# Optimization experiments

Hardware: AMD Instinct MI355X
Metric: run time of the kernel (lower is better)

Reference implementation:

```python
import jax, jax.numpy as jnp
import numpy as np

B, L, DIM = 16, 131072, 9  # batch, audio samples, 1 fundamental + 8 harmonics
SR = 22050.0
SINE_AMP = 0.1
NOISE_STD = 0.003


def setup_inputs() -> dict:
    key = jax.random.key(0)
    k1, k2, k3, k4 = jax.random.split(key, 4)
    u = jax.random.uniform(k1, (B, L, 1), dtype=jnp.float32)
    voiced = jax.random.uniform(k2, (B, L, 1), dtype=jnp.float32) > 0.3
    f0 = jnp.where(voiced, 100.0 + 300.0 * u, 0.0)  # Hz, 0 where unvoiced
    rand_ini = jax.random.uniform(k3, (B, DIM), dtype=jnp.float32)
    rand_ini = rand_ini.at[:, 0].set(0.0)  # first harmonic gets no random phase
    noise_z = jax.random.normal(k4, (B, L, DIM), dtype=jnp.float32)
    return {"f0": f0, "rand_ini": rand_ini, "noise_z": noise_z}


def reference(f0, rand_ini, noise_z):
    dim = noise_z.shape[-1]
    two_pi = 2.0 * jnp.pi
    # harmonic multiples of f0: (B, L, dim)
    k = jnp.arange(1, dim + 1, dtype=f0.dtype)
    fn = f0 * k
    # normalized per-step phase increment in [0, 1)
    rad = jnp.mod(fn / SR, 1.0)
    rad = rad.at[:, 0, :].add(rand_ini)  # random initial phase per harmonic
    # wrap-around detection: cumulative phase mod 1 decreases at a wrap
    tmp_over_one = jnp.mod(jnp.cumsum(rad, axis=1), 1.0)
    wrap = (tmp_over_one[:, 1:, :] - tmp_over_one[:, :-1, :]) < 0.0
    cumsum_shift = jnp.concatenate(
        [jnp.zeros_like(rad[:, :1, :]), jnp.where(wrap, -1.0, 0.0).astype(rad.dtype)],
        axis=1,
    )
    sines = jnp.sin(jnp.cumsum(rad + cumsum_shift, axis=1) * two_pi)
    sine_waves = sines * SINE_AMP
    # voiced/unvoiced mask from fundamental f0
    uv = (f0 > 0.0).astype(f0.dtype)  # (B, L, 1)
    noise_amp = uv * NOISE_STD + (1.0 - uv) * (SINE_AMP / 3.0)
    noise = noise_amp * noise_z
    sine_waves = sine_waves * uv + noise
    return sine_waves, uv, noise
```

## Files before the change

### kernel.cpp

```cpp
#include <hip/hip_runtime.h>
#include <math.h>


#define Bq 16
#define Lq 131072
#define DIMq 9
#define CHUNK 2048
#define NCHUNK (Lq / CHUNK)
#define NTHREADS 256
#define PER_THREAD (CHUNK / NTHREADS)

static __device__ __forceinline__ int pad9(int p) { return p + (p >> 3); }

__global__ void __launch_bounds__(NTHREADS) k_partials(
    const float* __restrict__ f0, double* __restrict__ part) {
  int b = blockIdx.x / NCHUNK, c = blockIdx.x % NCHUNK;
  const float* p = f0 + (size_t)b * Lq + (size_t)c * CHUNK;
  double s = 0.0;
#pragma unroll
  for (int j = 0; j < PER_THREAD; ++j) s += (double)p[j * NTHREADS + threadIdx.x];
  __shared__ double sd[NTHREADS];
  sd[threadIdx.x] = s;
  __syncthreads();
  for (int off = NTHREADS / 2; off > 0; off >>= 1) {
    if (threadIdx.x < off) sd[threadIdx.x] += sd[threadIdx.x + off];
    __syncthreads();
  }
  if (threadIdx.x == 0) part[blockIdx.x] = sd[0];
}

__global__ void k_scan(double* __restrict__ part) {
  if (threadIdx.x == 0) {
    double run = 0.0;
    double* p = part + (size_t)blockIdx.x * NCHUNK;
    for (int c = 0; c < NCHUNK; ++c) { double v = p[c]; p[c] = run; run += v; }
  }
}

__global__ void __launch_bounds__(NTHREADS) k_main(
    const float* __restrict__ f0, const float* __restrict__ rini,
    const float* __restrict__ nz, const double* __restrict__ pref,
    float* __restrict__ out0, float* __restrict__ out1, float* __restrict__ out2) {
  int b = blockIdx.x / NCHUNK, c = blockIdx.x % NCHUNK;
  int tid = threadIdx.x;
  size_t rowbase = (size_t)b * Lq + (size_t)c * CHUNK;

  __shared__ float f0s[CHUNK + CHUNK / 8];
  __shared__ double Cl[CHUNK + CHUNK / 8];
  __shared__ double sd[NTHREADS];

#pragma unroll
  for (int j = 0; j < PER_THREAD; ++j) {
    int p = j * NTHREADS + tid;
    f0s[pad9(p)] = f0[rowbase + p];
  }
  __syncthreads();

  double run = 0.0;
  double inc[PER_THREAD];
#pragma unroll
  for (int j = 0; j < PER_THREAD; ++j) {
    run += (double)f0s[pad9(tid * PER_THREAD + j)];
    inc[j] = run;
  }
  sd[tid] = run;
  __syncthreads();
#pragma unroll
  for (int off = 1; off < NTHREADS; off <<= 1) {
    double v = (tid >= off) ? sd[tid - off] : 0.0;
    __syncthreads();
    sd[tid] += v;
    __syncthreads();
  }
  double base = pref[blockIdx.x] + (sd[tid] - run);
#pragma unroll
  for (int j = 0; j < PER_THREAD; ++j)
    Cl[pad9(tid * PER_THREAD + j)] = base + inc[j];
  __syncthreads();

  float ini[DIMq];
#pragma unroll
  for (int d = 0; d < DIMq; ++d) ini[d] = rini[b * DIMq + d];

  const double invsr = 1.0 / 22050.0;
  const float nampU = (float)(0.1 / 3.0);

  for (int j = 0; j < PER_THREAD; ++j) {
    int p = j * NTHREADS + tid;
    size_t t = rowbase + p;
    float f = f0s[pad9(p)];
    bool v = f > 0.0f;
    out1[t] = v ? 1.0f : 0.0f;
    double x = Cl[pad9(p)] * invsr;
    float namp = v ? 0.003f : nampU;
    const float* nzp = nz + t * DIMq;
    float* o0 = out0 + t * DIMq;
    float* o2 = out2 + t * DIMq;
#pragma unroll
    for (int d = 0; d < DIMq; ++d) {
      float nzv = nzp[d];
      float noise = namp * nzv;
      double ph = x * (double)(d + 1) + (double)ini[d];
      ph -= floor(ph);
      float s = __builtin_amdgcn_sinf((float)ph) * 0.1f;
      o2[d] = noise;
      o0[d] = v ? (s + noise) : noise;
    }
  }
}

extern "C" void kernel_launch(void* const* d_in, const int* in_sizes, int n_in,
                              void* d_out, int out_size, void* d_ws, size_t ws_size,
                              hipStream_t stream) {
  const float* f0 = (const float*)d_in[0];
  const float* rini = (const float*)d_in[1];
  const float* nz = (const float*)d_in[2];
  float* out = (float*)d_out;
  float* out0 = out;
  float* out1 = out + (size_t)Bq * Lq * DIMq;
  float* out2 = out1 + (size_t)Bq * Lq;
  double* part = (double*)d_ws;

  k_partials<<<Bq * NCHUNK, NTHREADS, 0, stream>>>(f0, part);
  k_scan<<<Bq, 64, 0, stream>>>(part);
  k_main<<<Bq * NCHUNK, NTHREADS, 0, stream>>>(f0, rini, nz, part,
                                               out0, out1, out2);
}
```

Measured before the change: 53.97 us.

## Vectorize noise I/O, drop scan kernel, use wave shuffles and float harmonic phases

Removes the serial k_scan launch by having each k_main block sum the preceding chunk partials with a wave reduction. Block-level shared-memory scans and reductions become wave shuffles. Each per-sample phase is reduced mod 1 in double once, and the nine harmonic phases are then computed in float. The 9-wide noise input and both 9-wide outputs are read and written as coalesced float4 over a flat index instead of strided scalar accesses. The float harmonic-phase step reduces precision slightly, since the value multiplied by up to 9 is already a float.

```diff
diff --git a/kernel.cpp b/kernel.cpp
--- a/kernel.cpp
+++ b/kernel.cpp
@@ -7,105 +7,109 @@
 #define DIMq 9
 #define CHUNK 2048
 #define NCHUNK (Lq / CHUNK)
-#define NTHREADS 256
-#define PER_THREAD (CHUNK / NTHREADS)
+#define NT 256
+#define PT 8
+#define Q4 (CHUNK * DIMq / 4 / NT)
 
-static __device__ __forceinline__ int pad9(int p) { return p + (p >> 3); }
-
-__global__ void __launch_bounds__(NTHREADS) k_partials(
-    const float* __restrict__ f0, double* __restrict__ part) {
-  int b = blockIdx.x / NCHUNK, c = blockIdx.x % NCHUNK;
-  const float* p = f0 + (size_t)b * Lq + (size_t)c * CHUNK;
-  double s = 0.0;
+__global__ void __launch_bounds__(NT) k_partials(const float* __restrict__ f0,
+                                                 double* __restrict__ part) {
+  int b = blockIdx.x >> 6, tid = threadIdx.x, lane = tid & 63, wave = tid >> 6;
+  const float* p = f0 + (size_t)b * Lq + (size_t)(blockIdx.x & 63) * CHUNK + tid * PT;
+  float4 x = *(const float4*)p;
+  float4 y = *(const float4*)(p + 4);
+  double s = ((double)x.x + (double)x.y) + ((double)x.z + (double)x.w) +
+             ((double)y.x + (double)y.y) + ((double)y.z + (double)y.w);
 #pragma unroll
-  for (int j = 0; j < PER_THREAD; ++j) s += (double)p[j * NTHREADS + threadIdx.x];
-  __shared__ double sd[NTHREADS];
-  sd[threadIdx.x] = s;
+  for (int d = 32; d > 0; d >>= 1) s += __shfl_xor(s, d, 64);
+  __shared__ double ws[NT / 64];
+  if (lane == 0) ws[wave] = s;
   __syncthreads();
-  for (int off = NTHREADS / 2; off > 0; off >>= 1) {
-    if (threadIdx.x < off) sd[threadIdx.x] += sd[threadIdx.x + off];
-    __syncthreads();
-  }
-  if (threadIdx.x == 0) part[blockIdx.x] = sd[0];
+  if (tid == 0) part[blockIdx.x] = ws[0] + ws[1] + ws[2] + ws[3];
 }
 
-__global__ void k_scan(double* __restrict__ part) {
-  if (threadIdx.x == 0) {
-    double run = 0.0;
-    double* p = part + (size_t)blockIdx.x * NCHUNK;
-    for (int c = 0; c < NCHUNK; ++c) { double v = p[c]; p[c] = run; run += v; }
+__global__ void __launch_bounds__(NT) k_main(
+    const float* __restrict__ f0, const float* __restrict__ rini,
+    const float* __restrict__ nz, const double* __restrict__ part,
+    float* __restrict__ out0, float* __restrict__ out1,
+    float* __restrict__ out2) {
+  int bc = blockIdx.x;
+  int b = bc >> 6, c = bc & 63;
+  int tid = threadIdx.x, lane = tid & 63, wave = tid >> 6;
+  size_t t0g = (size_t)b * Lq + (size_t)c * CHUNK;
+
+  __shared__ float p1s[CHUNK + CHUNK / 8];
+  __shared__ float nmps[CHUNK + CHUNK / 8];
+  __shared__ float inis[DIMq];
+  __shared__ double wsum[NT / 64];
+
+  const float* fp = f0 + t0g + tid * PT;
+  float4 fa = *(const float4*)fp;
+  float4 fb = *(const float4*)(fp + 4);
+  float fv[PT] = {fa.x, fa.y, fa.z, fa.w, fb.x, fb.y, fb.z, fb.w};
+  double run = 0.0, inc[PT];
+#pragma unroll
+  for (int j = 0; j < PT; ++j) { run += (double)fv[j]; inc[j] = run; }
+  double tot = run;
+#pragma unroll
+  for (int d = 1; d < 64; d <<= 1) {
+    double o = __shfl_up(tot, d, 64);
+    if (lane >= d) tot += o;
   }
-}
-
-__global__ void __launch_bounds__(NTHREADS) k_main(
-    const float* __restrict__ f0, const float* __restrict__ rini,
-    const float* __restrict__ nz, const double* __restrict__ pref,
-    float* __restrict__ out0, float* __restrict__ out1, float* __restrict__ out2) {
-  int b = blockIdx.x / NCHUNK, c = blockIdx.x % NCHUNK;
-  int tid = threadIdx.x;
-  size_t rowbase = (size_t)b * Lq + (size_t)c * CHUNK;
-
-  __shared__ float f0s[CHUNK + CHUNK / 8];
-  __shared__ double Cl[CHUNK + CHUNK / 8];
-  __shared__ double sd[NTHREADS];
-
+  if (lane == 63) wsum[wave] = tot;
+  if (tid < DIMq) inis[tid] = rini[b * DIMq + tid];
+  __syncthreads();
+  double pv = (lane < c) ? part[(b << 6) + lane] : 0.0;
 #pragma unroll
-  for (int j = 0; j < PER_THREAD; ++j) {
-    int p = j * NTHREADS + tid;
-    f0s[pad9(p)] = f0[rowbase + p];
+  for (int d = 32; d > 0; d >>= 1) pv += __shfl_xor(pv, d, 64);
+  double wpre = 0.0;
+  for (int w = 0; w < wave; ++w) wpre += wsum[w];
+  double base = pv + wpre + (tot - run);
+  const double invsr = 1.0 / 22050.0;
+  const float nampU = (float)(0.1 / 3.0);
+  float uvv[PT];
+#pragma unroll
+  for (int j = 0; j < PT; ++j) {
+    double ph = (base + inc[j]) * invsr;
+    ph -= floor(ph);
+    int t = tid * PT + j;
+    p1s[t + (t >> 3)] = (float)ph;
+    bool v = fv[j] > 0.0f;
+    nmps[t + (t >> 3)] = v ? 0.003f : -nampU;
+    uvv[j] = v ? 1.0f : 0.0f;
   }
+  *(float4*)(out1 + t0g + tid * PT) = make_float4(uvv[0], uvv[1], uvv[2], uvv[3]);
+  *(float4*)(out1 + t0g + tid * PT + 4) = make_float4(uvv[4], uvv[5], uvv[6], uvv[7]);
   __syncthreads();
 
-  double run = 0.0;
-  double inc[PER_THREAD];
-#pragma unroll
-  for (int j = 0; j < PER_THREAD; ++j) {
-    run += (double)f0s[pad9(tid * PER_THREAD + j)];
-    inc[j] = run;
-  }
-  sd[tid] = run;
-  __syncthreads();
-#pragma unroll
-  for (int off = 1; off < NTHREADS; off <<= 1) {
-    double v = (tid >= off) ? sd[tid - off] : 0.0;
-    __syncthreads();
-    sd[tid] += v;
-    __syncthreads();
-  }
-  double base = pref[blockIdx.x] + (sd[tid] - run);
-#pragma unroll
-  for (int j = 0; j < PER_THREAD; ++j)
-    Cl[pad9(tid * PER_THREAD + j)] = base + inc[j];
-  __syncthreads();
+  const float4* nzc = (const float4*)(nz + t0g * DIMq);
+  float4* o0c = (float4*)(out0 + t0g * DIMq);
+  float4* o2c = (float4*)(out2 + t0g * DIMq);
 
-  float ini[DIMq];
-#pragma unroll
-  for (int d = 0; d < DIMq; ++d) ini[d] = rini[b * DIMq + d];
+  auto gen = [&](int t, int d, float nzv, float& r0, float& r2) {
+    int ti = t + (t >> 3);
+    float p1 = p1s[ti], nm = nmps[ti];
+    float ph = (float)(d + 1) * p1 + inis[d];
+    ph -= floorf(ph);
+    float s = __builtin_amdgcn_sinf(ph) * 0.1f;
+    float noise = fabsf(nm) * nzv;
+    r2 = noise;
+    r0 = (nm > 0.0f) ? s + noise : noise;
+  };
 
-  const double invsr = 1.0 / 22050.0;
-  const float nampU = (float)(0.1 / 3.0);
-
-  for (int j = 0; j < PER_THREAD; ++j) {
-    int p = j * NTHREADS + tid;
-    size_t t = rowbase + p;
-    float f = f0s[pad9(p)];
-    bool v = f > 0.0f;
-    out1[t] = v ? 1.0f : 0.0f;
-    double x = Cl[pad9(p)] * invsr;
-    float namp = v ? 0.003f : nampU;
-    const float* nzp = nz + t * DIMq;
-    float* o0 = out0 + t * DIMq;
-    float* o2 = out2 + t * DIMq;
-#pragma unroll
-    for (int d = 0; d < DIMq; ++d) {
-      float nzv = nzp[d];
-      float noise = namp * nzv;
-      double ph = x * (double)(d + 1) + (double)ini[d];
-      ph -= floor(ph);
-      float s = __builtin_amdgcn_sinf((float)ph) * 0.1f;
-      o2[d] = noise;
-      o0[d] = v ? (s + noise) : noise;
-    }
+#pragma unroll 6
+  for (int w = 0; w < Q4; ++w) {
+    int q = w * NT + tid;
+    int e = q * 4;
+    int t = (int)(((unsigned)e * 7282u) >> 16);
+    int d = e - t * 9;
+    float4 nzv = nzc[q];
+    float4 r0, r2;
+    gen(t, d, nzv.x, r0.x, r2.x); if (++d == 9) { d = 0; ++t; }
+    gen(t, d, nzv.y, r0.y, r2.y); if (++d == 9) { d = 0; ++t; }
+    gen(t, d, nzv.z, r0.z, r2.z); if (++d == 9) { d = 0; ++t; }
+    gen(t, d, nzv.w, r0.w, r2.w);
+    o0c[q] = r0;
+    o2c[q] = r2;
   }
 }
 
@@ -121,8 +125,6 @@
   float* out2 = out1 + (size_t)Bq * Lq;
   double* part = (double*)d_ws;
 
-  k_partials<<<Bq * NCHUNK, NTHREADS, 0, stream>>>(f0, part);
-  k_scan<<<Bq, 64, 0, stream>>>(part);
-  k_main<<<Bq * NCHUNK, NTHREADS, 0, stream>>>(f0, rini, nz, part,
-                                               out0, out1, out2);
+  k_partials<<<Bq * NCHUNK, NT, 0, stream>>>(f0, part);
+  k_main<<<Bq * NCHUNK, NT, 0, stream>>>(f0, rini, nz, part, out0, out1, out2);
 }
```

New measurement: 47.97 us. 1.13x faster.
